# Optimization experiments

Measured on AMD Instinct MI355X. Metric: run time of the kernel, lower is better.

## Reference

```python
import jax, jax.numpy as jnp
import numpy as np

N, D = 96, 512
EPS = 1e-8
INV_TEMP = 100.0  # 1 / 0.01


def _pair_indices(n):
    # all ordered pairs (i, j) with i != j, row-major like the original loops
    i, j = np.meshgrid(np.arange(n), np.arange(n), indexing='ij')
    mask = i != j
    return jnp.asarray(i[mask]), jnp.asarray(j[mask])


def setup_inputs() -> dict:
    key = jax.random.key(0)
    k1, k2 = jax.random.split(key)
    return {
        "txtf": jax.random.normal(k1, (N, D), dtype=jnp.float32),
        "imgf": jax.random.normal(k2, (N, D), dtype=jnp.float32),
    }


def reference(txtf, imgf):
    n = txtf.shape[0]
    ii, jj = _pair_indices(n)  # [P], P = n*(n-1)

    td = txtf[ii] - txtf[jj]                                   # [P, D]
    td = td / (jnp.linalg.norm(td, axis=-1, keepdims=True) + EPS)
    im = imgf[ii] - imgf[jj]                                   # [P, D]
    im = im / (jnp.linalg.norm(im, axis=-1, keepdims=True) + EPS)

    mma = jnp.einsum('pd,qd->pq', td, im) * INV_TEMP           # [P, P]
    diag = jnp.arange(mma.shape[0])
    # CE(mma, labels): softmax over rows; CE(mma.T, labels): softmax over cols
    lp_row = jax.nn.log_softmax(mma, axis=-1)
    lp_col = jax.nn.log_softmax(mma, axis=0)
    loss1 = -jnp.mean(lp_row[diag, diag])
    loss2 = -jnp.mean(lp_col[diag, diag])
    return (loss1 + loss2) * 0.5
```

## Files before the change

kernel.cpp:

```cpp
#include <hip/hip_runtime.h>
#include <math.h>

#define NN 96
#define DD 512
#define PP 9120
#define EPSF 1e-8f
#define INV_TEMP 100.0f
#define LOG2E 1.4426950408889634f
#define RT 8
#define NTASK (2*PP)
#define NBLK_T (NTASK/RT)
#define CBASE (PP/RT)
#define NPBLK 1152

#define OFF_G     0
#define OFF_GT    9216
#define OFF_WT    18432
#define OFF_WM    27648
#define OFF_WST   36864
#define OFF_WSM   46080
#define OFF_WMAXS 55296

__device__ __forceinline__ void decomp(unsigned p, int& i, int& j) {
    unsigned ii = p / 95u;
    unsigned r  = p - ii * 95u;
    i = (int)ii;
    j = (int)(r + (r >= ii ? 1u : 0u));
}

__device__ __forceinline__ float rdlane(float v, int srclane) {
    return __int_as_float(__builtin_amdgcn_readlane(__float_as_int(v), srclane));
}

__global__ __launch_bounds__(256) void prep_kernel(const float* __restrict__ txt,
                                                   const float* __restrict__ img,
                                                   float* __restrict__ ws) {
    __shared__ float wtw[4], wmw[4];
    int b = blockIdx.x, tid = threadIdx.x;
    int lane = tid & 63, wv = tid >> 6;
    const float4* T4 = (const float4*)txt;
    const float4* M4 = (const float4*)img;
    float bwt = 0.f, bwm = 0.f;

    #pragma unroll
    for (int q = 0; q < 2; ++q) {
        int pp = b * 8 + wv * 2 + q;
        int i = pp / NN, j = pp - i * NN;
        const float4* Ti = T4 + i * 128 + 2 * lane;
        const float4* Tj = T4 + j * 128 + 2 * lane;
        const float4* Mi = M4 + i * 128 + 2 * lane;
        const float4* Mj = M4 + j * 128 + 2 * lane;
        float gij = 0.f, nt2 = 0.f, nm2 = 0.f;
        #pragma unroll
        for (int u = 0; u < 2; ++u) {
            float4 a = Ti[u], t = Tj[u], c = Mi[u], d = Mj[u];
            gij += a.x*d.x + a.y*d.y + a.z*d.z + a.w*d.w;
            float d0 = a.x-t.x, d1 = a.y-t.y, d2 = a.z-t.z, d3 = a.w-t.w;
            nt2 += d0*d0 + d1*d1 + d2*d2 + d3*d3;
            float e0 = c.x-d.x, e1 = c.y-d.y, e2 = c.z-d.z, e3 = c.w-d.w;
            nm2 += e0*e0 + e1*e1 + e2*e2 + e3*e3;
        }
        #pragma unroll
        for (int off = 32; off > 0; off >>= 1) {
            gij += __shfl_xor(gij, off, 64);
            nt2 += __shfl_xor(nt2, off, 64);
            nm2 += __shfl_xor(nm2, off, 64);
        }
        float wt = 0.f, wm = 0.f;
        if (i != j) {
            wt = 1.f / (sqrtf(fmaxf(nt2, 0.f)) + EPSF);
            wm = 1.f / (sqrtf(fmaxf(nm2, 0.f)) + EPSF);
        }
        bwt = fmaxf(bwt, wt); bwm = fmaxf(bwm, wm);
        if (lane == 0) {
            int t0 = i * NN + j;
            ws[OFF_G  + t0] = gij;
            ws[OFF_GT + j * NN + i] = gij;
            ws[OFF_WT  + t0] = wt;
            ws[OFF_WM  + t0] = wm;
            ws[OFF_WST + t0] = wt * LOG2E;
            ws[OFF_WSM + t0] = wm * LOG2E;
        }
    }
    if (lane == 0) { wtw[wv] = bwt; wmw[wv] = bwm; }
    __syncthreads();
    if (tid == 0) {
        ws[OFF_WMAXS + b]         = fmaxf(fmaxf(wtw[0], wtw[1]), fmaxf(wtw[2], wtw[3]));
        ws[OFF_WMAXS + NPBLK + b] = fmaxf(fmaxf(wmw[0], wmw[1]), fmaxf(wmw[2], wmw[3]));
    }
}

__global__ __launch_bounds__(256) void lse_kernel(const float* __restrict__ ws,
                                                  float* __restrict__ out) {
    __shared__ float A[RT * NN];
    __shared__ float M2s[RT];
    __shared__ float Ms[RT];
    __shared__ float wred[4][RT];
    __shared__ float cred[RT];

    int tid = threadIdx.x, lane = tid & 63, wv = tid >> 6;
    int b = blockIdx.x;
    bool is_col = (b >= CBASE);
    const float* Mat    = ws + (is_col ? OFF_GT  : OFF_G);
    const float* wself  = ws + (is_col ? OFF_WM  : OFF_WT);
    const float* wsweep = ws + (is_col ? OFF_WST : OFF_WSM);

    const float* wmx = ws + OFF_WMAXS + (is_col ? 0 : NPBLK);
    float wl = 0.f;
    #pragma unroll
    for (int u = 0; u < 18; ++u)
        wl = fmaxf(wl, wmx[lane + 64 * u]);
    #pragma unroll
    for (int off = 32; off > 0; off >>= 1)
        wl = fmaxf(wl, __shfl_xor(wl, off, 64));
    float Wmax = wl;
    int base = (b - (is_col ? CBASE : 0)) * RT;

    #pragma unroll
    for (int q = 0; q < 2; ++q) {
        int rr = 2 * wv + q;
        int i, j; decomp((unsigned)(base + rr), i, j);
        float s = INV_TEMP * wself[i * NN + j];
        const float* Mi = Mat + i * NN;
        const float* Mj = Mat + j * NN;
        float v0 = s * (Mi[lane] - Mj[lane]);
        A[rr * NN + lane] = v0;
        float vmax = v0, vmin = v0;
        if (lane < 32) {
            float v1 = s * (Mi[64 + lane] - Mj[64 + lane]);
            A[rr * NN + 64 + lane] = v1;
            vmax = fmaxf(vmax, v1); vmin = fminf(vmin, v1);
        }
        #pragma unroll
        for (int off = 32; off > 0; off >>= 1) {
            vmax = fmaxf(vmax, __shfl_xor(vmax, off, 64));
            vmin = fminf(vmin, __shfl_xor(vmin, off, 64));
        }
        if (lane == 0) {
            float M = Wmax * (vmax - vmin);
            Ms[rr] = M;
            M2s[rr] = M * LOG2E;
        }
    }
    __syncthreads();

    int l1 = (lane < 32) ? (64 + lane) : (lane - 32);
    float M2[RT], aL1[RT], aL2[RT], S[RT];
    float a0r[RT], a1r[RT];
    #pragma unroll
    for (int r = 0; r < RT; ++r) {
        M2[r] = __int_as_float(__builtin_amdgcn_readfirstlane(__float_as_int(M2s[r])));
        a0r[r] = A[r * NN + lane];
        a1r[r] = A[r * NN + 64 + (lane & 31)];
        aL1[r] = A[r * NN + l1];
        aL2[r] = A[r * NN + lane + 32];
        S[r] = 0.f;
    }

    {
        int k0n = 2 * wv;
        float nw0 = wsweep[k0n * NN + lane];
        float nw1 = wsweep[(lane < 32 ? k0n : k0n + 1) * NN + l1];
        float nw2 = wsweep[(k0n + 1) * NN + lane + 32];
        #pragma unroll
        for (int u = 0; u < 12; ++u) {
            float w0 = nw0, w1 = nw1, w2 = nw2;
            if (u < 11) {
                int nk0 = 2 * (wv + 4 * (u + 1));
                nw0 = wsweep[nk0 * NN + lane];
                nw1 = wsweep[(lane < 32 ? nk0 : nk0 + 1) * NN + l1];
                nw2 = wsweep[(nk0 + 1) * NN + lane + 32];
            }
            #pragma unroll
            for (int r = 0; r < RT; ++r) {
                float akx, aky;
                if (u < 8) {
                    int sl = 2 * wv + 8 * u;
                    akx = rdlane(a0r[r], sl);
                    aky = rdlane(a0r[r], sl + 1);
                } else {
                    int sl = 2 * wv + 8 * (u - 8);
                    akx = rdlane(a1r[r], sl);
                    aky = rdlane(a1r[r], sl + 1);
                }
                float aksel = (lane < 32) ? akx : aky;
                S[r] += __builtin_amdgcn_exp2f(w0 * (akx   - a0r[r]) - M2[r])
                      + __builtin_amdgcn_exp2f(w1 * (aksel - aL1[r]) - M2[r])
                      + __builtin_amdgcn_exp2f(w2 * (aky   - aL2[r]) - M2[r]);
            }
        }
    }

    #pragma unroll
    for (int off = 32; off > 0; off >>= 1) {
        #pragma unroll
        for (int r = 0; r < RT; ++r) S[r] += __shfl_xor(S[r], off, 64);
    }
    if (lane == 0) {
        #pragma unroll
        for (int r = 0; r < RT; ++r) wred[wv][r] = S[r];
    }
    __syncthreads();

    if (tid < RT) {
        int r = tid;
        float tot = wred[0][r] + wred[1][r] + wred[2][r] + wred[3][r];
        tot -= 96.f * __builtin_amdgcn_exp2f(-M2s[r]);
        int i, j; decomp((unsigned)(base + r), i, j);
        float wtv = ws[OFF_WT + i * NN + j];
        float wmv = ws[OFF_WM + i * NN + j];
        float gii = ws[OFF_G + i * NN + i], gjj = ws[OFF_G + j * NN + j];
        float gij = ws[OFF_G + i * NN + j], gji = ws[OFF_G + j * NN + i];
        float dia = INV_TEMP * wtv * wmv * (gii - gij - gji + gjj);
        cred[r] = Ms[r] + logf(tot) - dia;
    }
    __syncthreads();
    if (tid == 0) {
        float c = 0.f;
        #pragma unroll
        for (int r = 0; r < RT; ++r) c += cred[r];
        atomicAdd(out, c * (1.0f / (float)NTASK));
    }
}

extern "C" void kernel_launch(void* const* d_in, const int* in_sizes, int n_in,
                              void* d_out, int out_size, void* d_ws, size_t ws_size,
                              hipStream_t stream) {
    const float* txt = (const float*)d_in[0];
    const float* img = (const float*)d_in[1];
    float* ws = (float*)d_ws;
    prep_kernel<<<NPBLK, 256, 0, stream>>>(txt, img, ws);
    lse_kernel<<<NBLK_T, 256, 0, stream>>>(ws, (float*)d_out);
}
```

Measured before the change: 99.23 us.

## Hoist global weight-max into separate kernel and loop LSE blocks over tasks

Adds a single-block kernel that reduces the per-block weight maxima once, so LSE blocks no longer each re-read and reduce 1152 partial maxima. The LSE kernel now launches 570 persistent-style blocks, each looping over 4 task groups of 8 rows, instead of 2280 blocks. This trades an extra kernel launch and serialized single-block reduction for less redundant work and fewer block launches. It also issues fewer concurrent blocks, which may reduce latency hiding.

New measurement: 128.1 us. 1.29x slower.

```diff
diff --git a/kernel.cpp b/kernel.cpp
--- a/kernel.cpp
+++ b/kernel.cpp
@@ -12,6 +12,8 @@
 #define NBLK_T (NTASK/RT)
 #define CBASE (PP/RT)
 #define NPBLK 1152
+#define GLSE 570
+#define NG 4
 
 #define OFF_G     0
 #define OFF_GT    9216
@@ -20,6 +22,7 @@
 #define OFF_WST   36864
 #define OFF_WSM   46080
 #define OFF_WMAXS 55296
+#define OFF_WMAXR 57600
 
 __device__ __forceinline__ void decomp(unsigned p, int& i, int& j) {
     unsigned ii = p / 95u;
@@ -90,6 +93,25 @@
     }
 }
 
+__global__ __launch_bounds__(256) void wmax_kernel(float* __restrict__ ws) {
+    __shared__ float ra[256], rb[256];
+    int tid = threadIdx.x;
+    float a = 0.f, m = 0.f;
+    for (int u = tid; u < NPBLK; u += 256) {
+        a = fmaxf(a, ws[OFF_WMAXS + u]);
+        m = fmaxf(m, ws[OFF_WMAXS + NPBLK + u]);
+    }
+    ra[tid] = a; rb[tid] = m; __syncthreads();
+    for (int t = 128; t > 0; t >>= 1) {
+        if (tid < t) {
+            ra[tid] = fmaxf(ra[tid], ra[tid + t]);
+            rb[tid] = fmaxf(rb[tid], rb[tid + t]);
+        }
+        __syncthreads();
+    }
+    if (tid == 0) { ws[OFF_WMAXR] = ra[0]; ws[OFF_WMAXR + 1] = rb[0]; }
+}
+
 __global__ __launch_bounds__(256) void lse_kernel(const float* __restrict__ ws,
                                                   float* __restrict__ out) {
     __shared__ float A[RT * NN];
@@ -100,126 +122,124 @@
 
     int tid = threadIdx.x, lane = tid & 63, wv = tid >> 6;
     int b = blockIdx.x;
-    bool is_col = (b >= CBASE);
-    const float* Mat    = ws + (is_col ? OFF_GT  : OFF_G);
-    const float* wself  = ws + (is_col ? OFF_WM  : OFF_WT);
-    const float* wsweep = ws + (is_col ? OFF_WST : OFF_WSM);
-
-    const float* wmx = ws + OFF_WMAXS + (is_col ? 0 : NPBLK);
-    float wl = 0.f;
-    #pragma unroll
-    for (int u = 0; u < 18; ++u)
-        wl = fmaxf(wl, wmx[lane + 64 * u]);
-    #pragma unroll
-    for (int off = 32; off > 0; off >>= 1)
-        wl = fmaxf(wl, __shfl_xor(wl, off, 64));
-    float Wmax = wl;
-    int base = (b - (is_col ? CBASE : 0)) * RT;
-
-    #pragma unroll
-    for (int q = 0; q < 2; ++q) {
-        int rr = 2 * wv + q;
-        int i, j; decomp((unsigned)(base + rr), i, j);
-        float s = INV_TEMP * wself[i * NN + j];
-        const float* Mi = Mat + i * NN;
-        const float* Mj = Mat + j * NN;
-        float v0 = s * (Mi[lane] - Mj[lane]);
-        A[rr * NN + lane] = v0;
-        float vmax = v0, vmin = v0;
-        if (lane < 32) {
-            float v1 = s * (Mi[64 + lane] - Mj[64 + lane]);
-            A[rr * NN + 64 + lane] = v1;
-            vmax = fmaxf(vmax, v1); vmin = fminf(vmin, v1);
-        }
+    int l1 = (lane < 32) ? (64 + lane) : (lane - 32);
+    const float wmaxT = ws[OFF_WMAXR];
+    const float wmaxM = ws[OFF_WMAXR + 1];
+
+    for (int g = 0; g < NG; ++g) {
+        int tb = g * GLSE + b;
+        bool is_col = (tb >= CBASE);
+        const float* Mat    = ws + (is_col ? OFF_GT  : OFF_G);
+        const float* wself  = ws + (is_col ? OFF_WM  : OFF_WT);
+        const float* wsweep = ws + (is_col ? OFF_WST : OFF_WSM);
+        float Wmax = is_col ? wmaxT : wmaxM;
+        int base = (tb - (is_col ? CBASE : 0)) * RT;
+
+        #pragma unroll
+        for (int q = 0; q < 2; ++q) {
+            int rr = 2 * wv + q;
+            int i, j; decomp((unsigned)(base + rr), i, j);
+            float s = INV_TEMP * wself[i * NN + j];
+            const float* Mi = Mat + i * NN;
+            const float* Mj = Mat + j * NN;
+            float v0 = s * (Mi[lane] - Mj[lane]);
+            A[rr * NN + lane] = v0;
+            float vmax = v0, vmin = v0;
+            if (lane < 32) {
+                float v1 = s * (Mi[64 + lane] - Mj[64 + lane]);
+                A[rr * NN + 64 + lane] = v1;
+                vmax = fmaxf(vmax, v1); vmin = fminf(vmin, v1);
+            }
+            #pragma unroll
+            for (int off = 32; off > 0; off >>= 1) {
+                vmax = fmaxf(vmax, __shfl_xor(vmax, off, 64));
+                vmin = fminf(vmin, __shfl_xor(vmin, off, 64));
+            }
+            if (lane == 0) {
+                float M = Wmax * (vmax - vmin);
+                Ms[rr] = M;
+                M2s[rr] = M * LOG2E;
+            }
+        }
+        __syncthreads();
+
+        float M2[RT], aL1[RT], aL2[RT], S[RT];
+        float a0r[RT], a1r[RT];
+        #pragma unroll
+        for (int r = 0; r < RT; ++r) {
+            M2[r] = __int_as_float(__builtin_amdgcn_readfirstlane(__float_as_int(M2s[r])));
+            a0r[r] = A[r * NN + lane];
+            a1r[r] = A[r * NN + 64 + (lane & 31)];
+            aL1[r] = A[r * NN + l1];
+            aL2[r] = A[r * NN + lane + 32];
+            S[r] = 0.f;
+        }
+
+        {
+            int k0n = 2 * wv;
+            float nw0 = wsweep[k0n * NN + lane];
+            float nw1 = wsweep[(lane < 32 ? k0n : k0n + 1) * NN + l1];
+            float nw2 = wsweep[(k0n + 1) * NN + lane + 32];
+            #pragma unroll
+            for (int u = 0; u < 12; ++u) {
+                float w0 = nw0, w1 = nw1, w2 = nw2;
+                if (u < 11) {
+                    int nk0 = 2 * (wv + 4 * (u + 1));
+                    nw0 = wsweep[nk0 * NN + lane];
+                    nw1 = wsweep[(lane < 32 ? nk0 : nk0 + 1) * NN + l1];
+                    nw2 = wsweep[(nk0 + 1) * NN + lane + 32];
+                }
+                #pragma unroll
+                for (int r = 0; r < RT; ++r) {
+                    float akx, aky;
+                    if (u < 8) {
+                        int sl = 2 * wv + 8 * u;
+                        akx = rdlane(a0r[r], sl);
+                        aky = rdlane(a0r[r], sl + 1);
+                    } else {
+                        int sl = 2 * wv + 8 * (u - 8);
+                        akx = rdlane(a1r[r], sl);
+                        aky = rdlane(a1r[r], sl + 1);
+                    }
+                    float aksel = (lane < 32) ? akx : aky;
+                    S[r] += __builtin_amdgcn_exp2f(w0 * (akx   - a0r[r]) - M2[r])
+                          + __builtin_amdgcn_exp2f(w1 * (aksel - aL1[r]) - M2[r])
+                          + __builtin_amdgcn_exp2f(w2 * (aky   - aL2[r]) - M2[r]);
+                }
+            }
+        }
+
         #pragma unroll
         for (int off = 32; off > 0; off >>= 1) {
-            vmax = fmaxf(vmax, __shfl_xor(vmax, off, 64));
-            vmin = fminf(vmin, __shfl_xor(vmin, off, 64));
+            #pragma unroll
+            for (int r = 0; r < RT; ++r) S[r] += __shfl_xor(S[r], off, 64);
         }
         if (lane == 0) {
-            float M = Wmax * (vmax - vmin);
-            Ms[rr] = M;
-            M2s[rr] = M * LOG2E;
-        }
-    }
-    __syncthreads();
-
-    int l1 = (lane < 32) ? (64 + lane) : (lane - 32);
-    float M2[RT], aL1[RT], aL2[RT], S[RT];
-    float a0r[RT], a1r[RT];
-    #pragma unroll
-    for (int r = 0; r < RT; ++r) {
-        M2[r] = __int_as_float(__builtin_amdgcn_readfirstlane(__float_as_int(M2s[r])));
-        a0r[r] = A[r * NN + lane];
-        a1r[r] = A[r * NN + 64 + (lane & 31)];
-        aL1[r] = A[r * NN + l1];
-        aL2[r] = A[r * NN + lane + 32];
-        S[r] = 0.f;
-    }
-
-    {
-        int k0n = 2 * wv;
-        float nw0 = wsweep[k0n * NN + lane];
-        float nw1 = wsweep[(lane < 32 ? k0n : k0n + 1) * NN + l1];
-        float nw2 = wsweep[(k0n + 1) * NN + lane + 32];
-        #pragma unroll
-        for (int u = 0; u < 12; ++u) {
-            float w0 = nw0, w1 = nw1, w2 = nw2;
-            if (u < 11) {
-                int nk0 = 2 * (wv + 4 * (u + 1));
-                nw0 = wsweep[nk0 * NN + lane];
-                nw1 = wsweep[(lane < 32 ? nk0 : nk0 + 1) * NN + l1];
-                nw2 = wsweep[(nk0 + 1) * NN + lane + 32];
-            }
-            #pragma unroll
-            for (int r = 0; r < RT; ++r) {
-                float akx, aky;
-                if (u < 8) {
-                    int sl = 2 * wv + 8 * u;
-                    akx = rdlane(a0r[r], sl);
-                    aky = rdlane(a0r[r], sl + 1);
-                } else {
-                    int sl = 2 * wv + 8 * (u - 8);
-                    akx = rdlane(a1r[r], sl);
-                    aky = rdlane(a1r[r], sl + 1);
-                }
-                float aksel = (lane < 32) ? akx : aky;
-                S[r] += __builtin_amdgcn_exp2f(w0 * (akx   - a0r[r]) - M2[r])
-                      + __builtin_amdgcn_exp2f(w1 * (aksel - aL1[r]) - M2[r])
-                      + __builtin_amdgcn_exp2f(w2 * (aky   - aL2[r]) - M2[r]);
-            }
-        }
-    }
-
-    #pragma unroll
-    for (int off = 32; off > 0; off >>= 1) {
-        #pragma unroll
-        for (int r = 0; r < RT; ++r) S[r] += __shfl_xor(S[r], off, 64);
-    }
-    if (lane == 0) {
-        #pragma unroll
-        for (int r = 0; r < RT; ++r) wred[wv][r] = S[r];
-    }
-    __syncthreads();
-
-    if (tid < RT) {
-        int r = tid;
-        float tot = wred[0][r] + wred[1][r] + wred[2][r] + wred[3][r];
-        tot -= 96.f * __builtin_amdgcn_exp2f(-M2s[r]);
-        int i, j; decomp((unsigned)(base + r), i, j);
-        float wtv = ws[OFF_WT + i * NN + j];
-        float wmv = ws[OFF_WM + i * NN + j];
-        float gii = ws[OFF_G + i * NN + i], gjj = ws[OFF_G + j * NN + j];
-        float gij = ws[OFF_G + i * NN + j], gji = ws[OFF_G + j * NN + i];
-        float dia = INV_TEMP * wtv * wmv * (gii - gij - gji + gjj);
-        cred[r] = Ms[r] + logf(tot) - dia;
-    }
-    __syncthreads();
-    if (tid == 0) {
-        float c = 0.f;
-        #pragma unroll
-        for (int r = 0; r < RT; ++r) c += cred[r];
-        atomicAdd(out, c * (1.0f / (float)NTASK));
+            #pragma unroll
+            for (int r = 0; r < RT; ++r) wred[wv][r] = S[r];
+        }
+        __syncthreads();
+
+        if (tid < RT) {
+            int r = tid;
+            float tot = wred[0][r] + wred[1][r] + wred[2][r] + wred[3][r];
+            tot -= 96.f * __builtin_amdgcn_exp2f(-M2s[r]);
+            int i, j; decomp((unsigned)(base + r), i, j);
+            float wtv = ws[OFF_WT + i * NN + j];
+            float wmv = ws[OFF_WM + i * NN + j];
+            float gii = ws[OFF_G + i * NN + i], gjj = ws[OFF_G + j * NN + j];
+            float gij = ws[OFF_G + i * NN + j], gji = ws[OFF_G + j * NN + i];
+            float dia = INV_TEMP * wtv * wmv * (gii - gij - gji + gjj);
+            cred[r] = Ms[r] + logf(tot) - dia;
+        }
+        __syncthreads();
+        if (tid == 0) {
+            float c = 0.f;
+            #pragma unroll
+            for (int r = 0; r < RT; ++r) c += cred[r];
+            atomicAdd(out, c * (1.0f / (float)NTASK));
+        }
+        __syncthreads();
     }
 }
 
@@ -230,5 +250,6 @@
     const float* img = (const float*)d_in[1];
     float* ws = (float*)d_ws;
     prep_kernel<<<NPBLK, 256, 0, stream>>>(txt, img, ws);
-    lse_kernel<<<NBLK_T, 256, 0, stream>>>(ws, (float*)d_out);
-}
+    wmax_kernel<<<1, 256, 0, stream>>>(ws);
+    lse_kernel<<<GLSE, 256, 0, stream>>>(ws, (float*)d_out);
+}
```
